# Kernel tuning notes

Measured on AMD Instinct MI355X. Metric: run time of the kernel, lower is better.

Reference implementation:

```python
import jax, jax.numpy as jnp
import numpy as np

SEQ_LEN = 1000
IN_DIM = 100
POOL = SEQ_LEN // IN_DIM  # 10
HIDDEN = 64
OUT_DIM = 5
N_BASIS = 16
BATCH = 65536


def setup_inputs() -> dict:
    key = jax.random.key(0)
    k1, k2, k3 = jax.random.split(key, 3)
    x = jax.random.normal(k1, (BATCH, SEQ_LEN), dtype=jnp.float32)
    c1_mu = jax.random.normal(k2, (HIDDEN, IN_DIM, N_BASIS), dtype=jnp.float32) * 0.05
    c2_mu = jax.random.normal(k3, (OUT_DIM, HIDDEN, N_BASIS), dtype=jnp.float32) * 0.05
    centers = jnp.linspace(-3.0, 3.0, N_BASIS, dtype=jnp.float32)
    return {"x": x, "c1_mu": c1_mu, "c2_mu": c2_mu, "centers": centers}


def _norm(x):
    # torch .std() uses ddof=1 (unbiased)
    mu = jnp.mean(x, axis=1, keepdims=True)
    sd = jnp.std(x, axis=1, keepdims=True, ddof=1)
    return (x - mu) / (sd + 1e-6)


def _basis(x, centers):
    # x: [b, d] -> [b, d, n_basis]; RBF with fixed variance 0.36
    d = x[..., None] - centers
    return jnp.exp(-0.5 * d * d / 0.36)


def _kan(x, c, centers):
    B = _basis(x, centers)  # [b, i, n]
    return jnp.einsum('bin,oin->bo', B, c)


def reference(x, c1_mu, c2_mu, centers):
    b = x.shape[0]
    # unfold(1, pool, pool).mean(-1): non-overlapping average pooling
    x = x.reshape(b, IN_DIM, POOL).mean(-1)  # [b, 100]
    x = _norm(x)
    h = jnp.tanh(_kan(x, c1_mu, centers))  # [b, 64]
    h = _norm(h)
    out = _kan(h, c2_mu, centers)  # [b, 5]
    return out
```

## Files before the change

kernel.cpp:

```cpp
#include <hip/hip_runtime.h>
#include <hip/hip_bf16.h>


#define SEQ    1000
#define INDIM  100
#define HID    64
#define OUTD   5
#define ROWS   16
#define NTHR   128

typedef __bf16 v8bf __attribute__((ext_vector_type(8)));
typedef float  v4f  __attribute__((ext_vector_type(4)));

#define XSTR 101
#define HSTR 65
#define RSTR 68
#define R2STR 20

#if __has_builtin(__builtin_amdgcn_exp2f)
#define EXP2(x) __builtin_amdgcn_exp2f(x)
#else
#define EXP2(x) exp2f(x)
#endif
#if __has_builtin(__builtin_amdgcn_rcpf)
#define RCP(x) __builtin_amdgcn_rcpf(x)
#else
#define RCP(x) (1.f / (x))
#endif
#if __has_builtin(__builtin_amdgcn_sqrtf)
#define SQRT(x) __builtin_amdgcn_sqrtf(x)
#else
#define SQRT(x) sqrtf(x)
#endif

__global__ __launch_bounds__(256) void cvt_w(
    const float* __restrict__ c1, const float* __restrict__ c2,
    __bf16* __restrict__ c1p, __bf16* __restrict__ c2p)
{
  int t = blockIdx.x * 256 + threadIdx.x;
  if (t < 12800) {
    int lane = t & 63, frag = t >> 6;
    int cb = frag & 3, ks = frag >> 2;
    int l15 = lane & 15, q = lane >> 4;
    const float4* s = (const float4*)(c1 + (size_t)(cb * 16 + l15) * 1600 + ks * 32 + q * 8);
    float4 v0 = s[0], v1 = s[1];
    __bf16* d = c1p + (size_t)t * 8;
    d[0]=(__bf16)v0.x; d[1]=(__bf16)v0.y; d[2]=(__bf16)v0.z; d[3]=(__bf16)v0.w;
    d[4]=(__bf16)v1.x; d[5]=(__bf16)v1.y; d[6]=(__bf16)v1.z; d[7]=(__bf16)v1.w;
  }
  if (t < 2048) {
    int lane = t & 63, t8 = t >> 6;
    int row = lane & 15, q = lane >> 4;
    __bf16* d = c2p + (size_t)t * 8;
    if (row < OUTD) {
      const float4* s = (const float4*)(c2 + (size_t)row * 1024 + t8 * 32 + q * 8);
      float4 v0 = s[0], v1 = s[1];
      d[0]=(__bf16)v0.x; d[1]=(__bf16)v0.y; d[2]=(__bf16)v0.z; d[3]=(__bf16)v0.w;
      d[4]=(__bf16)v1.x; d[5]=(__bf16)v1.y; d[6]=(__bf16)v1.z; d[7]=(__bf16)v1.w;
    } else {
      #pragma unroll
      for (int j = 0; j < 8; ++j) d[j] = (__bf16)0.f;
    }
  }
}

#define MFMA __builtin_amdgcn_mfma_f32_16x16x32_bf16

__global__ __launch_bounds__(NTHR, 6) void kan_main(
    const float* __restrict__ x, const __bf16* __restrict__ c1p,
    const __bf16* __restrict__ c2p, const float* __restrict__ cen,
    float* __restrict__ out)
{
  __shared__ __align__(16) float sm[2128];
  float* xn   = sm;
  float* red  = sm;
  float* hb   = sm + 1088;
  float* red2 = sm;

  const int tid  = threadIdx.x;
  const int w    = tid >> 6, lane = tid & 63;
  const int row0 = blockIdx.x * ROWS;
  const int l15 = lane & 15, q = lane >> 4, iq = q >> 1;

  const float Sn2 = 1.41553628f;
  const float TL2 = 2.88539008f;
  float cs[8];
  {
    const int n0 = (q & 1) * 8;
    #pragma unroll
    for (int j = 0; j < 8; ++j) cs[j] = cen[n0 + j] * Sn2;
  }

  const int pr   = (w << 3) + (lane >> 3);
  const int slot = lane & 7;
  float pva[14];
  float s = 0.f, s2 = 0.f;
  {
    const float* xg = x + (size_t)(row0 + pr) * SEQ;
    #pragma unroll
    for (int it = 0; it < 7; ++it) {
      int p = slot + (it << 3);
      float u0 = 0.f, u1 = 0.f;
      if (p < 50) {
        const float4* xp = (const float4*)(xg + p * 20);
        float4 a0 = xp[0], a1 = xp[1], a2 = xp[2], a3 = xp[3], a4 = xp[4];
        u0 = a0.x+a0.y+a0.z+a0.w + a1.x+a1.y+a1.z+a1.w + a2.x+a2.y;
        u1 = a2.z+a2.w + a3.x+a3.y+a3.z+a3.w + a4.x+a4.y+a4.z+a4.w;
        s += u0 + u1; s2 += u0*u0 + u1*u1;
      }
      pva[2*it] = u0; pva[2*it+1] = u1;
    }
  }
  #pragma unroll
  for (int m = 1; m <= 4; m <<= 1) {
    s += __shfl_xor(s, m, 64); s2 += __shfl_xor(s2, m, 64);
  }
  {
    float mu  = s * 0.01f;
    float var = (s2 - 100.f * mu * mu) * (1.f / 99.f);
    float rs  = Sn2 * RCP(SQRT(fmaxf(var, 0.f)) + 1e-5f);
    #pragma unroll
    for (int it = 0; it < 7; ++it) {
      int p = slot + (it << 3);
      if (p < 50) {
        xn[pr * XSTR + 2*p]     = (pva[2*it]     - mu) * rs;
        xn[pr * XSTR + 2*p + 1] = (pva[2*it + 1] - mu) * rs;
      }
    }
  }
  __syncthreads();

  const float* xr = xn + l15 * XSTR;
  const __bf16* bp = c1p + (size_t)(51200 * w) + lane * 8;
  v4f acc[4];
  acc[0] = (v4f){0.f,0.f,0.f,0.f}; acc[1] = acc[0]; acc[2] = acc[0]; acc[3] = acc[0];

  v8bf bA0 = *(const v8bf*)(bp +    0);
  v8bf bA1 = *(const v8bf*)(bp +  512);
  v8bf bA2 = *(const v8bf*)(bp + 1024);
  v8bf bA3 = *(const v8bf*)(bp + 1536);
  bp += 2048;

  #pragma unroll
  for (int c5 = 0; c5 < 5; ++c5) {
    const int c = w * 5 + c5;
    float xv[5];
    #pragma unroll
    for (int k = 0; k < 5; ++k) xv[k] = xr[c * 10 + 2 * k + iq];
    #pragma unroll
    for (int ks = 0; ks < 5; ++ks) {
      v8bf nb0, nb1, nb2, nb3;
      if (c5 * 5 + ks < 24) {
        nb0 = *(const v8bf*)(bp +    0);
        nb1 = *(const v8bf*)(bp +  512);
        nb2 = *(const v8bf*)(bp + 1024);
        nb3 = *(const v8bf*)(bp + 1536);
      }
      bp += 2048;
      v8bf a;
      {
        float xvk = xv[ks];
        #pragma unroll
        for (int j = 0; j < 8; ++j) {
          float d = xvk - cs[j];
          a[j] = (__bf16)EXP2(-(d * d));
        }
      }
      acc[0] = MFMA(a, bA0, acc[0], 0, 0, 0);
      acc[1] = MFMA(a, bA1, acc[1], 0, 0, 0);
      acc[2] = MFMA(a, bA2, acc[2], 0, 0, 0);
      acc[3] = MFMA(a, bA3, acc[3], 0, 0, 0);
      if (c5 * 5 + ks < 24) { bA0 = nb0; bA1 = nb1; bA2 = nb2; bA3 = nb3; }
    }
  }
  __syncthreads();

  #pragma unroll
  for (int rgo = 0; rgo < 2; ++rgo) {
    int rg = 2 * (1 - w) + rgo;
    #pragma unroll
    for (int cb = 0; cb < 4; ++cb)
      red[(q * 4 + rg) * RSTR + cb * 16 + l15] = acc[cb][rg];
  }
  __syncthreads();
  #pragma unroll
  for (int rgo = 0; rgo < 2; ++rgo) {
    int rg = 2 * w + rgo;
    float h[4], ss = 0.f, ss2 = 0.f;
    #pragma unroll
    for (int cb = 0; cb < 4; ++cb) {
      float t = acc[cb][rg] + red[(q * 4 + rg) * RSTR + cb * 16 + l15];
      float e = EXP2(t * TL2);
      float hv = 1.f - 2.f * RCP(e + 1.f);
      h[cb] = hv; ss += hv; ss2 += hv * hv;
    }
    #pragma unroll
    for (int m = 1; m <= 8; m <<= 1) {
      ss += __shfl_xor(ss, m, 64); ss2 += __shfl_xor(ss2, m, 64);
    }
    float muh  = ss * (1.f / 64.f);
    float varh = (ss2 - 64.f * muh * muh) * (1.f / 63.f);
    float rsh  = Sn2 * RCP(SQRT(fmaxf(varh, 0.f)) + 1e-6f);
    #pragma unroll
    for (int cb = 0; cb < 4; ++cb)
      hb[(q * 4 + rg) * HSTR + cb * 16 + l15] = (h[cb] - muh) * rsh;
  }
  __syncthreads();

  const float* hr = hb + l15 * HSTR;
  float hv16[16];
  #pragma unroll
  for (int t = 0; t < 16; ++t) hv16[t] = hr[2 * (16 * w + t) + iq];
  const __bf16* bp2 = c2p + (size_t)(16 * w) * 512 + lane * 8;
  v8bf vb = *(const v8bf*)(bp2);
  v4f o4 = (v4f){0.f, 0.f, 0.f, 0.f};
  #pragma unroll
  for (int t = 0; t < 16; ++t) {
    v8bf nvb;
    if (t < 15) nvb = *(const v8bf*)(bp2 + (t + 1) * 512);
    v8bf a;
    {
      float hvv = hv16[t];
      #pragma unroll
      for (int j = 0; j < 8; ++j) {
        float d = hvv - cs[j];
        a[j] = (__bf16)EXP2(-(d * d));
      }
    }
    o4 = MFMA(a, vb, o4, 0, 0, 0);
    if (t < 15) vb = nvb;
  }
  if (w == 0) {
    #pragma unroll
    for (int rg = 0; rg < 4; ++rg)
      red2[(q * 4 + rg) * R2STR + l15] = o4[rg];
  }
  __syncthreads();
  if (w == 1 && l15 < OUTD) {
    #pragma unroll
    for (int rg = 0; rg < 4; ++rg) {
      int r = q * 4 + rg;
      out[(size_t)(row0 + r) * OUTD + l15] = o4[rg] + red2[r * R2STR + l15];
    }
  }
}

extern "C" void kernel_launch(void* const* d_in, const int* in_sizes, int n_in,
                              void* d_out, int out_size, void* d_ws, size_t ws_size,
                              hipStream_t stream) {
  const float* x   = (const float*)d_in[0];
  const float* c1  = (const float*)d_in[1];
  const float* c2  = (const float*)d_in[2];
  const float* cen = (const float*)d_in[3];
  float* out = (float*)d_out;

  __bf16* c1p = (__bf16*)d_ws;
  __bf16* c2p = (__bf16*)((char*)d_ws + 204800);

  hipLaunchKernelGGL(cvt_w, dim3(50), dim3(256), 0, stream, c1, c2, c1p, c2p);
  hipLaunchKernelGGL(kan_main, dim3(65536 / ROWS), dim3(NTHR), 0, stream,
                     x, c1p, c2p, cen, out);
}
```

Measured before the change: 401.0 us.

## Split pooling and normalization into a separate kernel feeding the KAN kernel

Moves the input average-pooling and row normalization out of the main KAN kernel into a dedicated pool_norm kernel that writes normalized rows to workspace. The main kernel then loads the compact 100-float rows with vectorized float4 loads into shared memory, which has a padded stride of 104. The aim is to separate the bandwidth-bound read of the large input from the MFMA-heavy compute, so each kernel can reach better occupancy and memory throughput. The cost is an extra launch plus a global round trip of 26 MB of normalized data, and larger shared memory use per block.

```diff
diff --git a/kernel.cpp b/kernel.cpp
--- a/kernel.cpp
+++ b/kernel.cpp
@@ -12,7 +12,7 @@
 typedef __bf16 v8bf __attribute__((ext_vector_type(8)));
 typedef float  v4f  __attribute__((ext_vector_type(4)));
 
-#define XSTR 101
+#define XSTR 104
 #define HSTR 65
 #define RSTR 68
 #define R2STR 20
@@ -64,35 +64,15 @@
   }
 }
 
-#define MFMA __builtin_amdgcn_mfma_f32_16x16x32_bf16
-
-__global__ __launch_bounds__(NTHR, 6) void kan_main(
-    const float* __restrict__ x, const __bf16* __restrict__ c1p,
-    const __bf16* __restrict__ c2p, const float* __restrict__ cen,
-    float* __restrict__ out)
+__global__ __launch_bounds__(256, 4) void pool_norm(
+    const float* __restrict__ x, float* __restrict__ xnb)
 {
-  __shared__ __align__(16) float sm[2128];
-  float* xn   = sm;
-  float* red  = sm;
-  float* hb   = sm + 1088;
-  float* red2 = sm;
-
   const int tid  = threadIdx.x;
-  const int w    = tid >> 6, lane = tid & 63;
-  const int row0 = blockIdx.x * ROWS;
-  const int l15 = lane & 15, q = lane >> 4, iq = q >> 1;
-
+  const int row0 = blockIdx.x * 32;
+  const int pr   = tid >> 3;
+  const int slot = tid & 7;
   const float Sn2 = 1.41553628f;
-  const float TL2 = 2.88539008f;
-  float cs[8];
-  {
-    const int n0 = (q & 1) * 8;
-    #pragma unroll
-    for (int j = 0; j < 8; ++j) cs[j] = cen[n0 + j] * Sn2;
-  }
-
-  const int pr   = (w << 3) + (lane >> 3);
-  const int slot = lane & 7;
+
   float pva[14];
   float s = 0.f, s2 = 0.f;
   {
@@ -115,17 +95,56 @@
   for (int m = 1; m <= 4; m <<= 1) {
     s += __shfl_xor(s, m, 64); s2 += __shfl_xor(s2, m, 64);
   }
+  float mu  = s * 0.01f;
+  float var = (s2 - 100.f * mu * mu) * (1.f / 99.f);
+  float rs  = Sn2 * RCP(SQRT(fmaxf(var, 0.f)) + 1e-5f);
+  float* xo = xnb + (size_t)(row0 + pr) * INDIM;
+  #pragma unroll
+  for (int it = 0; it < 7; ++it) {
+    int p = slot + (it << 3);
+    if (p < 50) {
+      float2 v2;
+      v2.x = (pva[2*it]     - mu) * rs;
+      v2.y = (pva[2*it + 1] - mu) * rs;
+      *(float2*)(xo + 2 * p) = v2;
+    }
+  }
+}
+
+#define MFMA __builtin_amdgcn_mfma_f32_16x16x32_bf16
+
+__global__ __launch_bounds__(NTHR, 6) void kan_main(
+    const float* __restrict__ xnb, const __bf16* __restrict__ c1p,
+    const __bf16* __restrict__ c2p, const float* __restrict__ cen,
+    float* __restrict__ out)
+{
+  __shared__ __align__(16) float sm[2704];
+  float* xn   = sm;
+  float* red  = sm;
+  float* hb   = sm + 1664;
+  float* red2 = sm;
+
+  const int tid  = threadIdx.x;
+  const int w    = tid >> 6, lane = tid & 63;
+  const int row0 = blockIdx.x * ROWS;
+  const int l15 = lane & 15, q = lane >> 4, iq = q >> 1;
+
+  const float Sn2 = 1.41553628f;
+  const float TL2 = 2.88539008f;
+  float cs[8];
   {
-    float mu  = s * 0.01f;
-    float var = (s2 - 100.f * mu * mu) * (1.f / 99.f);
-    float rs  = Sn2 * RCP(SQRT(fmaxf(var, 0.f)) + 1e-5f);
-    #pragma unroll
-    for (int it = 0; it < 7; ++it) {
-      int p = slot + (it << 3);
-      if (p < 50) {
-        xn[pr * XSTR + 2*p]     = (pva[2*it]     - mu) * rs;
-        xn[pr * XSTR + 2*p + 1] = (pva[2*it + 1] - mu) * rs;
-      }
+    const int n0 = (q & 1) * 8;
+    #pragma unroll
+    for (int j = 0; j < 8; ++j) cs[j] = cen[n0 + j] * Sn2;
+  }
+
+  #pragma unroll
+  for (int it = 0; it < 4; ++it) {
+    int idx = tid + it * NTHR;
+    if (idx < 400) {
+      int r = idx / 25, q4 = idx - r * 25;
+      float4 v = *(const float4*)(xnb + (size_t)(row0 + r) * INDIM + q4 * 4);
+      *(float4*)(xn + r * XSTR + q4 * 4) = v;
     }
   }
   __syncthreads();
@@ -256,8 +275,10 @@
 
   __bf16* c1p = (__bf16*)d_ws;
   __bf16* c2p = (__bf16*)((char*)d_ws + 204800);
+  float*  xnb = (float*)((char*)d_ws + 237568);
 
   hipLaunchKernelGGL(cvt_w, dim3(50), dim3(256), 0, stream, c1, c2, c1p, c2p);
+  hipLaunchKernelGGL(pool_norm, dim3(65536 / 32), dim3(256), 0, stream, x, xnb);
   hipLaunchKernelGGL(kan_main, dim3(65536 / ROWS), dim3(NTHR), 0, stream,
-                     x, c1p, c2p, cen, out);
-}
+                     xnb, c1p, c2p, cen, out);
+}
```

New measurement: 416.7 us. 1.04x slower.
